# Kernel optimization log

Measured on AMD Instinct MI355X. Metric: run time of the kernel, lower is better.

The kernel has to match this reference:

```python
import jax, jax.numpy as jnp
import numpy as np

N_WIRES = 4
DIM = 16  # 2**N_WIRES

# PauliZ eigenvalue signs per wire per basis state (wire 0 = MSB, torchquantum convention)
_Z = np.array([[1.0 - 2.0 * ((i >> (N_WIRES - 1 - w)) & 1) for i in range(DIM)]
               for w in range(N_WIRES)], dtype=np.float32)  # [4,16]

def _cnot_perm(c, t):
    mc = 1 << (N_WIRES - 1 - c)
    mt = 1 << (N_WIRES - 1 - t)
    return np.array([i ^ mt if (i & mc) else i for i in range(DIM)])

_PERM_WRAP = [_cnot_perm(0, 1), _cnot_perm(1, 2), _cnot_perm(2, 3), _cnot_perm(3, 0)]  # QLSTM ladder
_PERM_LINE = [_cnot_perm(0, 1), _cnot_perm(1, 2), _cnot_perm(2, 3)]                   # kernel ladder

def _apply_rx(state, theta, wire):
    """Apply RX(theta) on `wire`. state: [B,16] complex64. theta: scalar or [B]."""
    theta = jnp.asarray(theta)
    c = jnp.cos(theta / 2).astype(jnp.complex64)
    s = jnp.sin(theta / 2).astype(jnp.complex64)
    left = 2 ** wire
    right = 2 ** (N_WIRES - 1 - wire)
    st = state.reshape(-1, left, 2, right)
    a, b = st[:, :, 0, :], st[:, :, 1, :]
    if theta.ndim != 0:
        c = c[:, None, None]
        s = s[:, None, None]
    na = c * a - 1j * s * b
    nb = -1j * s * a + c * b
    return jnp.stack([na, nb], axis=2).reshape(-1, DIM)

def _circuit(angles, params, perms):
    """angles: [B,4] encoding RX angles; params: [4] trainable RX angles."""
    B = angles.shape[0]
    state = jnp.zeros((B, DIM), jnp.complex64).at[:, 0].set(1.0)
    for w in range(N_WIRES):
        state = _apply_rx(state, angles[:, w], w)
    for w in range(N_WIRES):
        state = _apply_rx(state, params[w], w)
    for p in perms:
        state = state[:, p]
    return state

def _measure_z(state):
    probs = state.real ** 2 + state.imag ** 2  # [B,16]
    return probs @ jnp.asarray(_Z).T           # [B,4]

def setup_inputs() -> dict:
    key = jax.random.key(0)
    ks = jax.random.split(key, 16)
    T, B, D, S, H = 128, 64, 32, 1024, 4
    inp = {
        'x': jax.random.normal(ks[0], (T, B, D), jnp.float32),
        'support_vectors': jax.random.normal(ks[1], (S, D), jnp.float32),
        'Wf': jax.random.normal(ks[2], (H, D + H), jnp.float32) * 0.1,
        'bf': jax.random.normal(ks[3], (H,), jnp.float32) * 0.1,
        'Wi': jax.random.normal(ks[4], (H, D + H), jnp.float32) * 0.1,
        'bi': jax.random.normal(ks[5], (H,), jnp.float32) * 0.1,
        'Wu': jax.random.normal(ks[6], (H, D + H), jnp.float32) * 0.1,
        'bu': jax.random.normal(ks[7], (H,), jnp.float32) * 0.1,
        'Wo': jax.random.normal(ks[8], (H, D + H), jnp.float32) * 0.1,
        'bo': jax.random.normal(ks[9], (H,), jnp.float32) * 0.1,
        'pf': jax.random.normal(ks[10], (H,), jnp.float32),
        'pi': jax.random.normal(ks[11], (H,), jnp.float32),
        'pu': jax.random.normal(ks[12], (H,), jnp.float32),
        'po': jax.random.normal(ks[13], (H,), jnp.float32),
        'qk_params': jax.random.normal(ks[14], (H,), jnp.float32),
    }
    return inp

def reference(x, support_vectors, Wf, bf, Wi, bi, Wu, bu, Wo, bo, pf, pi, pu, po, qk_params):
    T, B, D = x.shape
    gamma = 1.0
    xf = x.reshape(T * B, D)

    # classical RBF Gram matrix (materializes [N,S,D] diff, as in the original)
    diff = xf[:, None, :] - support_vectors[None, :, :]
    rbf = jnp.exp(-gamma * jnp.sum(diff * diff, axis=-1))  # [N,S]

    # quantum kernel: encode first 4 features, trainable RX, linear CNOT ladder
    sx = _circuit(xf[:, :4], qk_params, _PERM_LINE)               # [N,16] complex
    sy = _circuit(support_vectors[:, :4], qk_params, _PERM_LINE)  # [S,16] complex
    qk = jnp.abs(sx @ sy.T)  # no conjugation, matching torch.matmul(states_x, states_y.t())

    def gate(comb, W, b, p):
        return _measure_z(_circuit(comb @ W.T + b, p, _PERM_WRAP))

    def step(carry, xt):
        hx, cx = carry
        comb = jnp.concatenate([xt, hx], axis=1)
        f = jax.nn.sigmoid(gate(comb, Wf, bf, pf))
        i = jax.nn.sigmoid(gate(comb, Wi, bi, pi))
        g = jnp.tanh(gate(comb, Wu, bu, pu))
        o = jax.nn.sigmoid(gate(comb, Wo, bo, po))
        cx = f * cx + i * g
        hx = o * jnp.tanh(cx)
        return (hx, cx), hx

    h0 = jnp.zeros((B, N_WIRES), jnp.float32)
    c0 = jnp.zeros((B, N_WIRES), jnp.float32)
    (_, _), outs = jax.lax.scan(step, (h0, c0), x)  # outs: [T,B,4]
    return (outs, rbf, qk)
```

## Files before the change

kernel.cpp:

```cpp
#include <hip/hip_runtime.h>

#define T_STEPS 128
#define BATCH   64
#define DIMX    32
#define S_SUP   1024
#define NROW    8192
#define OUT_H_SZ   (T_STEPS*BATCH*4)
#define OUT_RBF_SZ (NROW*S_SUP)

__device__ __forceinline__ float rcp_fast(float x) { return __builtin_amdgcn_rcpf(x); }

template<int K>
__device__ __forceinline__ float quad_bcast(float v) {
    constexpr int ctrl = K * 0x55;
    return __builtin_bit_cast(float,
        __builtin_amdgcn_mov_dpp(__builtin_bit_cast(int, v), ctrl, 0xF, 0xF, true));
}

__global__ __launch_bounds__(256) void pre_kernel(
    const float* __restrict__ x,
    const float* __restrict__ Wf, const float* __restrict__ bf,
    const float* __restrict__ Wi, const float* __restrict__ bi,
    const float* __restrict__ Wu, const float* __restrict__ bu,
    const float* __restrict__ Wo, const float* __restrict__ bo,
    const float* __restrict__ pf, const float* __restrict__ pi,
    const float* __restrict__ pu, const float* __restrict__ po,
    float* __restrict__ pre)
{
    const int tid = threadIdx.x;
    const int rl  = tid >> 4;
    const int gw  = tid & 15;
    const int g   = gw >> 2, w = gw & 3;
    const int row = blockIdx.x * 16 + rl;

    __shared__ float xs[16 * DIMX];
    if (tid < 128) {
        ((float4*)xs)[tid] = ((const float4*)(x + (size_t)blockIdx.x * 16 * DIMX))[tid];
    }
    __syncthreads();

    const float* W  = (g == 0) ? Wf : (g == 1) ? Wi : (g == 2) ? Wu : Wo;
    const float* bb = (g == 0) ? bf : (g == 1) ? bi : (g == 2) ? bu : bo;
    const float* pp = (g == 0) ? pf : (g == 1) ? pi : (g == 2) ? pu : po;

    float acc = bb[w] + pp[w];
    const float* Wr = W + w * 36;
    const float* xr = xs + rl * DIMX;
#pragma unroll
    for (int d = 0; d < DIMX; d++) acc += xr[d] * Wr[d];

    pre[(row * 4 + g) * 4 + w] = acc;
}

__global__ __launch_bounds__(256) void fused_kernel(
    const float* __restrict__ x,  const float* __restrict__ sv,
    const float* __restrict__ Wf, const float* __restrict__ bf,
    const float* __restrict__ Wi, const float* __restrict__ bi,
    const float* __restrict__ Wu, const float* __restrict__ bu,
    const float* __restrict__ Wo, const float* __restrict__ bo,
    const float* __restrict__ pf, const float* __restrict__ pi,
    const float* __restrict__ pu, const float* __restrict__ po,
    const float* __restrict__ qkp, const float* __restrict__ pre,
    float* __restrict__ out_h, float* __restrict__ out_rbf, float* __restrict__ out_qk)
{
    __shared__ float xs[BATCH * DIMX];
    __shared__ float xn2[BATCH];
    const int tid = threadIdx.x;

    if (blockIdx.x == 0) {
        __builtin_amdgcn_s_setprio(3);
        const int b = tid >> 2, g = tid & 3;
        const float* W = (g == 0) ? Wf : (g == 1) ? Wi : (g == 2) ? Wu : Wo;

        float Wh[4][4];
#pragma unroll
        for (int w = 0; w < 4; w++)
#pragma unroll
            for (int j = 0; j < 4; j++) Wh[w][j] = W[w * 36 + 32 + j];

        const float kexp = (g == 2) ? -2.f : -1.f;
        const float Aa   = (g == 2) ?  2.f :  1.f;
        const float Bb   = (g == 2) ? -1.f :  0.f;
        const bool  isg1 = (g == 1), isg2 = (g == 2), isg3 = (g == 3);

        float h0 = 0.f, h1 = 0.f, h2 = 0.f, h3 = 0.f;
        float c0 = 0.f, c1 = 0.f, c2 = 0.f, c3 = 0.f;
        const int base = b * 4 + g;
        const float4* prep = (const float4*)pre;

        auto lstm_step = [&](int t, float4 cur) {
            float a0 = cur.x, a1 = cur.y, a2 = cur.z, a3 = cur.w;
            a0 += h0 * Wh[0][0] + h1 * Wh[0][1] + h2 * Wh[0][2] + h3 * Wh[0][3];
            a1 += h0 * Wh[1][0] + h1 * Wh[1][1] + h2 * Wh[1][2] + h3 * Wh[1][3];
            a2 += h0 * Wh[2][0] + h1 * Wh[2][1] + h2 * Wh[2][2] + h3 * Wh[2][3];
            a3 += h0 * Wh[3][0] + h1 * Wh[3][1] + h2 * Wh[3][2] + h3 * Wh[3][3];

            float C0 = __cosf(a0), C1 = __cosf(a1), C2 = __cosf(a2), C3 = __cosf(a3);
            float t23 = C2 * C3;
            float m01 = C0 * C1;
            float r0 = C1 * t23;
            float r1 = m01;
            float r2 = m01 * C2;
            float r3 = m01 * t23;

            float o0 = Aa * rcp_fast(1.f + __expf(r0 * kexp)) + Bb;
            float o1 = Aa * rcp_fast(1.f + __expf(r1 * kexp)) + Bb;
            float o2 = Aa * rcp_fast(1.f + __expf(r2 * kexp)) + Bb;
            float o3 = Aa * rcp_fast(1.f + __expf(r3 * kexp)) + Bb;

            float f0 = quad_bcast<0>(o0), f1 = quad_bcast<0>(o1), f2 = quad_bcast<0>(o2), f3 = quad_bcast<0>(o3);
            float i0 = quad_bcast<1>(o0), i1 = quad_bcast<1>(o1), i2 = quad_bcast<1>(o2), i3 = quad_bcast<1>(o3);
            float u0 = quad_bcast<2>(o0), u1 = quad_bcast<2>(o1), u2 = quad_bcast<2>(o2), u3 = quad_bcast<2>(o3);
            float z0 = quad_bcast<3>(o0), z1 = quad_bcast<3>(o1), z2 = quad_bcast<3>(o2), z3 = quad_bcast<3>(o3);

            c0 = f0 * c0 + i0 * u0;
            c1 = f1 * c1 + i1 * u1;
            c2 = f2 * c2 + i2 * u2;
            c3 = f3 * c3 + i3 * u3;

            float t0 = 2.f * rcp_fast(1.f + __expf(-2.f * c0)) - 1.f;
            float t1 = 2.f * rcp_fast(1.f + __expf(-2.f * c1)) - 1.f;
            float t2 = 2.f * rcp_fast(1.f + __expf(-2.f * c2)) - 1.f;
            float t3 = 2.f * rcp_fast(1.f + __expf(-2.f * c3)) - 1.f;
            h0 = z0 * t0; h1 = z1 * t1; h2 = z2 * t2; h3 = z3 * t3;

            float hsel = isg1 ? h1 : h0;
            hsel = isg2 ? h2 : hsel;
            hsel = isg3 ? h3 : hsel;
            out_h[t * 256 + tid] = hsel;
        };

        float4 cb0, cb1, cb2, cb3, cb4, cb5, cb6, cb7;
        cb0 = prep[base];           cb1 = prep[base + 256];
        cb2 = prep[base + 512];     cb3 = prep[base + 768];
        cb4 = prep[base + 1024];    cb5 = prep[base + 1280];
        cb6 = prep[base + 1536];    cb7 = prep[base + 1792];

#pragma unroll 1
        for (int tt = 0; tt < T_STEPS; tt += 8) {
            int nb = tt + 8; nb = (nb > T_STEPS - 8) ? (T_STEPS - 8) : nb;
            const float4* pc = prep + base + nb * 256;
            float4 nb0 = pc[0];
            float4 nb1 = pc[256];
            float4 nb2 = pc[512];
            float4 nb3 = pc[768];
            float4 nb4 = pc[1024];
            float4 nb5 = pc[1280];
            float4 nb6 = pc[1536];
            float4 nb7 = pc[1792];
            __builtin_amdgcn_sched_barrier(0);

            lstm_step(tt + 0, cb0);
            lstm_step(tt + 1, cb1);
            lstm_step(tt + 2, cb2);
            lstm_step(tt + 3, cb3);
            lstm_step(tt + 4, cb4);
            lstm_step(tt + 5, cb5);
            lstm_step(tt + 6, cb6);
            lstm_step(tt + 7, cb7);

            cb0 = nb0; cb1 = nb1; cb2 = nb2; cb3 = nb3;
            cb4 = nb4; cb5 = nb5; cb6 = nb6; cb7 = nb7;
        }
    } else {
        const int bid = blockIdx.x - 1;
        const int n0  = (bid >> 2) * BATCH;
        const int s0  = (bid & 3) * 256;

        float4* xs4 = (float4*)xs;
        const float4* xg = (const float4*)(x + (size_t)n0 * DIMX);
        float4 t0v = xg[tid];
        float4 t1v = xg[tid + 256];
        xs4[tid]       = t0v;
        xs4[tid + 256] = t1v;

        float p0 = t0v.x * t0v.x + t0v.y * t0v.y + t0v.z * t0v.z + t0v.w * t0v.w;
        float p1 = t1v.x * t1v.x + t1v.y * t1v.y + t1v.z * t1v.z + t1v.w * t1v.w;
        p0 += __shfl_xor(p0, 1); p1 += __shfl_xor(p1, 1);
        p0 += __shfl_xor(p0, 2); p1 += __shfl_xor(p1, 2);
        p0 += __shfl_xor(p0, 4); p1 += __shfl_xor(p1, 4);
        if ((tid & 7) == 0) {
            xn2[tid >> 3]        = p0;
            xn2[(tid >> 3) + 32] = p1;
        }

        const int s = s0 + tid;
        float4 svv[8];
        const float4* svg = (const float4*)(sv + (size_t)s * DIMX);
#pragma unroll
        for (int k = 0; k < 8; k++) svv[k] = svg[k];
        float sn2 = 0.f;
#pragma unroll
        for (int k = 0; k < 8; k++)
            sn2 += svv[k].x * svv[k].x + svv[k].y * svv[k].y + svv[k].z * svv[k].z + svv[k].w * svv[k].w;

        const float B0 = 0.5f * svv[0].x + qkp[0];
        const float B1 = 0.5f * svv[0].y + qkp[1];
        const float B2 = 0.5f * svv[0].z + qkp[2];
        const float B3 = 0.5f * svv[0].w + qkp[3];
        __syncthreads();

#pragma unroll 4
        for (int n = 0; n < BATCH; n++) {
            const float4* xr4 = (const float4*)(xs + n * DIMX);
            float4 xv0 = xr4[0];
            float dot = xv0.x * svv[0].x + xv0.y * svv[0].y + xv0.z * svv[0].z + xv0.w * svv[0].w;
#pragma unroll
            for (int k = 1; k < 8; k++) {
                float4 xv = xr4[k];
                dot += xv.x * svv[k].x + xv.y * svv[k].y + xv.z * svv[k].z + xv.w * svv[k].w;
            }
            float dist = xn2[n] + sn2 - 2.f * dot;
            float rb   = __expf(-dist);

            float qv = __cosf(0.5f * xv0.x + B0) * __cosf(0.5f * xv0.y + B1)
                     * __cosf(0.5f * xv0.z + B2) * __cosf(0.5f * xv0.w + B3);
            qv = fabsf(qv);

            const int row = n0 + n;
            out_rbf[(size_t)row * S_SUP + s] = rb;
            out_qk [(size_t)row * S_SUP + s] = qv;
        }
    }
}

extern "C" void kernel_launch(void* const* d_in, const int* in_sizes, int n_in,
                              void* d_out, int out_size, void* d_ws, size_t ws_size,
                              hipStream_t stream)
{
    const float* x   = (const float*)d_in[0];
    const float* sv  = (const float*)d_in[1];
    const float* Wf  = (const float*)d_in[2];
    const float* bf  = (const float*)d_in[3];
    const float* Wi  = (const float*)d_in[4];
    const float* bi  = (const float*)d_in[5];
    const float* Wu  = (const float*)d_in[6];
    const float* bu  = (const float*)d_in[7];
    const float* Wo  = (const float*)d_in[8];
    const float* bo  = (const float*)d_in[9];
    const float* pf  = (const float*)d_in[10];
    const float* pi  = (const float*)d_in[11];
    const float* pu  = (const float*)d_in[12];
    const float* po  = (const float*)d_in[13];
    const float* qkp = (const float*)d_in[14];

    float* out     = (float*)d_out;
    float* out_h   = out;
    float* out_rbf = out + OUT_H_SZ;
    float* out_qk  = out + OUT_H_SZ + OUT_RBF_SZ;

    float* pre = (float*)d_ws;

    pre_kernel<<<NROW / 16, 256, 0, stream>>>(x, Wf, bf, Wi, bi, Wu, bu, Wo, bo,
                                              pf, pi, pu, po, pre);
    fused_kernel<<<1 + 512, 256, 0, stream>>>(
        x, sv, Wf, bf, Wi, bi, Wu, bu, Wo, bo, pf, pi, pu, po, qkp, pre,
        out_h, out_rbf, out_qk);
}
```

Baseline: 149.4 us.

## Split LSTM recurrence across 16 blocks and stage precomputed gates in LDS

The serial LSTM recurrence, previously handled by one 256-thread block, is split across 16 blocks, each owning 4 batch rows with 16 active lanes. The pre kernel writes its gate pre-activations in a layout grouped by block, so each block bulk-loads its whole 128-step slice into shared memory before the loop. Each step then reads its inputs from LDS instead of global memory. The aim is to shorten the latency-bound serial critical path and take global loads off it. The cost is 16 blocks kept busy with mostly idle lanes and a larger shared-memory footprint for the RBF blocks.

```diff
diff --git a/kernel.cpp b/kernel.cpp
--- a/kernel.cpp
+++ b/kernel.cpp
@@ -7,6 +7,7 @@
 #define NROW    8192
 #define OUT_H_SZ   (T_STEPS*BATCH*4)
 #define OUT_RBF_SZ (NROW*S_SUP)
+#define N_LSTM_BLK 16
 
 __device__ __forceinline__ float rcp_fast(float x) { return __builtin_amdgcn_rcpf(x); }
 
@@ -32,6 +33,8 @@
     const int gw  = tid & 15;
     const int g   = gw >> 2, w = gw & 3;
     const int row = blockIdx.x * 16 + rl;
+    const int t   = row >> 6;
+    const int b   = row & 63;
 
     __shared__ float xs[16 * DIMX];
     if (tid < 128) {
@@ -49,27 +52,31 @@
 #pragma unroll
     for (int d = 0; d < DIMX; d++) acc += xr[d] * Wr[d];
 
-    pre[(row * 4 + g) * 4 + w] = acc;
+    const size_t fidx = ((size_t)((b >> 2) * 128 + t) * 16 + (b & 3) * 4 + g) * 4 + w;
+    pre[fidx] = acc;
 }
 
 __global__ __launch_bounds__(256) void fused_kernel(
     const float* __restrict__ x,  const float* __restrict__ sv,
-    const float* __restrict__ Wf, const float* __restrict__ bf,
-    const float* __restrict__ Wi, const float* __restrict__ bi,
-    const float* __restrict__ Wu, const float* __restrict__ bu,
-    const float* __restrict__ Wo, const float* __restrict__ bo,
-    const float* __restrict__ pf, const float* __restrict__ pi,
-    const float* __restrict__ pu, const float* __restrict__ po,
+    const float* __restrict__ Wf, const float* __restrict__ Wi,
+    const float* __restrict__ Wu, const float* __restrict__ Wo,
     const float* __restrict__ qkp, const float* __restrict__ pre,
     float* __restrict__ out_h, float* __restrict__ out_rbf, float* __restrict__ out_qk)
 {
-    __shared__ float xs[BATCH * DIMX];
-    __shared__ float xn2[BATCH];
+    __shared__ float4 smem4[2064];
     const int tid = threadIdx.x;
 
-    if (blockIdx.x == 0) {
+    if (blockIdx.x < N_LSTM_BLK) {
+        const int k = blockIdx.x;
+        const float4* src = (const float4*)pre + (size_t)k * 2048;
+#pragma unroll
+        for (int i = 0; i < 8; i++)
+            smem4[i * 256 + tid] = src[i * 256 + tid];
+        __syncthreads();
+        if (tid >= 16) return;
+
         __builtin_amdgcn_s_setprio(3);
-        const int b = tid >> 2, g = tid & 3;
+        const int lane = tid, g = lane & 3;
         const float* W = (g == 0) ? Wf : (g == 1) ? Wi : (g == 2) ? Wu : Wo;
 
         float Wh[4][4];
@@ -85,10 +92,15 @@
 
         float h0 = 0.f, h1 = 0.f, h2 = 0.f, h3 = 0.f;
         float c0 = 0.f, c1 = 0.f, c2 = 0.f, c3 = 0.f;
-        const int base = b * 4 + g;
-        const float4* prep = (const float4*)pre;
-
-        auto lstm_step = [&](int t, float4 cur) {
+
+        float4 cur = smem4[lane];
+        float4 nxt = smem4[16 + lane];
+
+#pragma unroll 2
+        for (int t = 0; t < T_STEPS; t++) {
+            const int ta = (t + 2 > T_STEPS - 1) ? (T_STEPS - 1) : (t + 2);
+            float4 after = smem4[ta * 16 + lane];
+
             float a0 = cur.x, a1 = cur.y, a2 = cur.z, a3 = cur.w;
             a0 += h0 * Wh[0][0] + h1 * Wh[0][1] + h2 * Wh[0][2] + h3 * Wh[0][3];
             a1 += h0 * Wh[1][0] + h1 * Wh[1][1] + h2 * Wh[1][2] + h3 * Wh[1][3];
@@ -127,43 +139,14 @@
             float hsel = isg1 ? h1 : h0;
             hsel = isg2 ? h2 : hsel;
             hsel = isg3 ? h3 : hsel;
-            out_h[t * 256 + tid] = hsel;
-        };
-
-        float4 cb0, cb1, cb2, cb3, cb4, cb5, cb6, cb7;
-        cb0 = prep[base];           cb1 = prep[base + 256];
-        cb2 = prep[base + 512];     cb3 = prep[base + 768];
-        cb4 = prep[base + 1024];    cb5 = prep[base + 1280];
-        cb6 = prep[base + 1536];    cb7 = prep[base + 1792];
-
-#pragma unroll 1
-        for (int tt = 0; tt < T_STEPS; tt += 8) {
-            int nb = tt + 8; nb = (nb > T_STEPS - 8) ? (T_STEPS - 8) : nb;
-            const float4* pc = prep + base + nb * 256;
-            float4 nb0 = pc[0];
-            float4 nb1 = pc[256];
-            float4 nb2 = pc[512];
-            float4 nb3 = pc[768];
-            float4 nb4 = pc[1024];
-            float4 nb5 = pc[1280];
-            float4 nb6 = pc[1536];
-            float4 nb7 = pc[1792];
-            __builtin_amdgcn_sched_barrier(0);
-
-            lstm_step(tt + 0, cb0);
-            lstm_step(tt + 1, cb1);
-            lstm_step(tt + 2, cb2);
-            lstm_step(tt + 3, cb3);
-            lstm_step(tt + 4, cb4);
-            lstm_step(tt + 5, cb5);
-            lstm_step(tt + 6, cb6);
-            lstm_step(tt + 7, cb7);
-
-            cb0 = nb0; cb1 = nb1; cb2 = nb2; cb3 = nb3;
-            cb4 = nb4; cb5 = nb5; cb6 = nb6; cb7 = nb7;
+            out_h[t * 256 + k * 16 + lane] = hsel;
+
+            cur = nxt; nxt = after;
         }
     } else {
-        const int bid = blockIdx.x - 1;
+        float* xs  = (float*)smem4;
+        float* xn2 = (float*)(smem4 + 2048);
+        const int bid = blockIdx.x - N_LSTM_BLK;
         const int n0  = (bid >> 2) * BATCH;
         const int s0  = (bid & 3) * 256;
 
@@ -253,7 +236,7 @@
 
     pre_kernel<<<NROW / 16, 256, 0, stream>>>(x, Wf, bf, Wi, bi, Wu, bu, Wo, bo,
                                               pf, pi, pu, po, pre);
-    fused_kernel<<<1 + 512, 256, 0, stream>>>(
-        x, sv, Wf, bf, Wi, bi, Wu, bu, Wo, bo, pf, pi, pu, po, qkp, pre,
+    fused_kernel<<<N_LSTM_BLK + 512, 256, 0, stream>>>(
+        x, sv, Wf, Wi, Wu, Wo, qkp, pre,
         out_h, out_rbf, out_qk);
 }
```

Result: no change. 152.4 us (+2.0%).
